# Kernel tuning notes

Measured on AMD Instinct MI355X. Metric: run time of the kernel, lower is better.

The kernel has to match this reference:

```python
import jax, jax.numpy as jnp
import numpy as np

N = 100_000
E = 1_600_000
IN, HID, OUT, ED = 128, 128, 64, 16
NEG_SLOPE = 0.2  # PyG GATConv default leaky_relu slope


def segment_softmax(logits, seg, num_segments):
    m = jax.ops.segment_max(logits, seg, num_segments=num_segments)
    m = jnp.where(jnp.isfinite(m), m, 0.0)
    e = jnp.exp(logits - m[seg])
    s = jax.ops.segment_sum(e, seg, num_segments=num_segments)
    return e / (s[seg] + 1e-16)


def gat_conv(x, edge_index, W, a_src, a_dst, b, edge_attr=None, We=None, ae=None):
    """PyG GATConv, heads=1, add_self_loops=True, fill_value='mean'."""
    n = x.shape[0]
    h = x @ W  # [N, C]
    loop = jnp.arange(n, dtype=edge_index.dtype)
    src = jnp.concatenate([edge_index[0], loop])  # [E+N]
    dst = jnp.concatenate([edge_index[1], loop])
    alpha = (h * a_src).sum(-1)[src] + (h * a_dst).sum(-1)[dst]  # [E+N]
    if edge_attr is not None:
        # self-loop edge_attr filled with per-destination mean (PyG fill_value='mean')
        cnt = jax.ops.segment_sum(jnp.ones((edge_attr.shape[0],), edge_attr.dtype), edge_index[1], num_segments=n)
        mean_attr = jax.ops.segment_sum(edge_attr, edge_index[1], num_segments=n) / jnp.maximum(cnt, 1.0)[:, None]
        ea = jnp.concatenate([edge_attr, mean_attr], axis=0)  # [E+N, ED]
        alpha = alpha + (ea @ We) @ ae
    alpha = jax.nn.leaky_relu(alpha, NEG_SLOPE)
    alpha = segment_softmax(alpha, dst, n)
    out = jax.ops.segment_sum(alpha[:, None] * h[src], dst, num_segments=n)  # scatter-add
    return out + b


def setup_inputs() -> dict:
    key = jax.random.key(0)
    ks = iter(jax.random.split(key, 32))
    g = lambda shape, fan: (jax.random.normal(next(ks), shape, jnp.float32) * (1.0 / np.sqrt(fan)))
    inp = {
        "x": jax.random.normal(next(ks), (N, IN), jnp.float32),
        "edge_index": jax.random.randint(next(ks), (2, E), 0, N, jnp.int32),
        "edge_attr": jax.random.normal(next(ks), (E, ED), jnp.float32),
        # conv1 (no edge_attr)
        "W1": g((IN, HID), IN), "a1_src": g((HID,), HID), "a1_dst": g((HID,), HID), "b1": jnp.zeros((HID,), jnp.float32),
        # conv2 (with edge_attr)
        "W2": g((HID, HID), HID), "a2_src": g((HID,), HID), "a2_dst": g((HID,), HID), "b2": jnp.zeros((HID,), jnp.float32),
        "We2": g((ED, HID), ED), "ae2": g((HID,), HID),
        # initial residual linear
        "Wr": g((IN, HID), IN), "br": jnp.zeros((HID,), jnp.float32),
        # conv_mu
        "Wmu": g((HID, OUT), HID), "amu_src": g((OUT,), OUT), "amu_dst": g((OUT,), OUT), "bmu": jnp.zeros((OUT,), jnp.float32),
        "Wemu": g((ED, OUT), ED), "aemu": g((OUT,), OUT),
        # conv_logstd
        "Wls": g((HID, OUT), HID), "als_src": g((OUT,), OUT), "als_dst": g((OUT,), OUT), "bls": jnp.zeros((OUT,), jnp.float32),
        "Wels": g((ED, OUT), ED), "aels": g((OUT,), OUT),
    }
    return inp


def reference(x, edge_index, edge_attr,
              W1, a1_src, a1_dst, b1,
              W2, a2_src, a2_dst, b2, We2, ae2,
              Wr, br,
              Wmu, amu_src, amu_dst, bmu, Wemu, aemu,
              Wls, als_src, als_dst, bls, Wels, aels):
    h = jax.nn.relu(gat_conv(x, edge_index, W1, a1_src, a1_dst, b1))
    h = jax.nn.relu(gat_conv(h, edge_index, W2, a2_src, a2_dst, b2, edge_attr, We2, ae2))
    h = h + (x @ Wr + br)  # initial residual
    mu = gat_conv(h, edge_index, Wmu, amu_src, amu_dst, bmu, edge_attr, Wemu, aemu)
    logstd = gat_conv(h, edge_index, Wls, als_src, als_dst, bls, edge_attr, Wels, aels)
    return mu, logstd
```

## Files before the change

kernel.cpp:

```cpp
#include <hip/hip_runtime.h>

#define NN 100000
#define NE 1600000
#define BSH 9
#define NBUK 196

typedef __attribute__((ext_vector_type(8))) short bf16x8;
typedef __attribute__((ext_vector_type(4))) float f32x4;

__device__ __forceinline__ float wave_sum(float v){
  #pragma unroll
  for (int o = 32; o; o >>= 1) v += __shfl_xor(v, o, 64);
  return v;
}
__device__ __forceinline__ float bf2f(unsigned short x){
  return __uint_as_float(((unsigned)x) << 16);
}
__device__ __forceinline__ unsigned short f2bf(float f){
  unsigned u = __float_as_uint(f);
  return (unsigned short)((u + 0x7FFFu + ((u >> 16) & 1u)) >> 16);
}
__device__ __forceinline__ float rl_f(float v, int j){
  return __uint_as_float(__builtin_amdgcn_readlane(__float_as_uint(v), j));
}

__global__ void prep_w_kernel(const float* __restrict__ W1, const float* __restrict__ W2,
                              const float* __restrict__ Wr, const float* __restrict__ Wmu,
                              const float* __restrict__ Wls,
                              unsigned short* __restrict__ W1t, unsigned short* __restrict__ W2t,
                              unsigned short* __restrict__ Wrt, unsigned short* __restrict__ Wmlt){
  int b = blockIdx.x, t = threadIdx.x;
  for (int it = 0; it < 64; it++){
    int idx = it*256 + t;
    int k = idx >> 7, c = idx & 127;
    float v; unsigned short* dst;
    if (b == 0){ v = W1[k*128+c]; dst = W1t; }
    else if (b == 1){ v = W2[k*128+c]; dst = W2t; }
    else if (b == 2){ v = Wr[k*128+c]; dst = Wrt; }
    else { v = (c & 1) ? Wls[k*64 + (c>>1)] : Wmu[k*64 + (c>>1)]; dst = Wmlt; }
    dst[c*128 + k] = f2bf(v);
  }
}

__global__ void wvec_kernel(const float* __restrict__ We2, const float* __restrict__ ae2,
                            const float* __restrict__ Wemu, const float* __restrict__ aemu,
                            const float* __restrict__ Wels, const float* __restrict__ aels,
                            float* __restrict__ wv){
  int t = threadIdx.x;
  if (t < 16){
    float s = 0.f; for (int c = 0; c < 128; c++) s += We2[t*128+c]*ae2[c];
    wv[t] = s;
  } else if (t < 32){
    int k = t-16; float s = 0.f; for (int c = 0; c < 64; c++) s += Wemu[k*64+c]*aemu[c];
    wv[16+k] = s;
  } else if (t < 48){
    int k = t-32; float s = 0.f; for (int c = 0; c < 64; c++) s += Wels[k*64+c]*aels[c];
    wv[32+k] = s;
  }
}

__global__ void cast_x_kernel(const float* __restrict__ x, unsigned short* __restrict__ Xb){
  int i = blockIdx.x*256 + threadIdx.x;
  if (i >= NN*128/8) return;
  const float4* src = (const float4*)x + (size_t)i*2;
  float4 v0 = src[0], v1 = src[1];
  ushort4 o0 = make_ushort4(f2bf(v0.x), f2bf(v0.y), f2bf(v0.z), f2bf(v0.w));
  ushort4 o1 = make_ushort4(f2bf(v1.x), f2bf(v1.y), f2bf(v1.z), f2bf(v1.w));
  *(ushort4*)(Xb + (size_t)i*8)     = o0;
  *(ushort4*)(Xb + (size_t)i*8 + 4) = o1;
}

__global__ void edge_scalar_kernel(const float* __restrict__ ea, const float* __restrict__ wv,
                                   float4* __restrict__ ew3){
  int e = blockIdx.x*256 + threadIdx.x;
  if (e >= NE) return;
  const float4* p = (const float4*)(ea + (size_t)e*16);
  float a[16]; float4 v;
  v = p[0]; a[0]=v.x; a[1]=v.y; a[2]=v.z; a[3]=v.w;
  v = p[1]; a[4]=v.x; a[5]=v.y; a[6]=v.z; a[7]=v.w;
  v = p[2]; a[8]=v.x; a[9]=v.y; a[10]=v.z; a[11]=v.w;
  v = p[3]; a[12]=v.x; a[13]=v.y; a[14]=v.z; a[15]=v.w;
  float s2 = 0.f, smu = 0.f, sls = 0.f;
  #pragma unroll
  for (int k = 0; k < 16; k++){
    s2  = fmaf(a[k], wv[k],    s2);
    smu = fmaf(a[k], wv[16+k], smu);
    sls = fmaf(a[k], wv[32+k], sls);
  }
  ew3[e] = make_float4(s2, smu, sls, 0.f);
}

__global__ void zero_kernel(int* __restrict__ p, int n){
  int i = blockIdx.x*256 + threadIdx.x;
  if (i < n) p[i] = 0;
}

__global__ __launch_bounds__(1024) void ehist_kernel(const int* __restrict__ ei,
                                                     unsigned* __restrict__ gbcnt){
  __shared__ unsigned h[256];
  int t = threadIdx.x;
  if (t < 256) h[t] = 0;
  __syncthreads();
  int e0 = blockIdx.x*4096 + t;
  #pragma unroll
  for (int k = 0; k < 4; k++){
    int e = e0 + k*1024;
    if (e < NE) atomicAdd(&h[ei[NE+e] >> BSH], 1);
  }
  __syncthreads();
  if (t < 256 && h[t]) atomicAdd(&gbcnt[t], h[t]);
}

__global__ void bscan_kernel(const unsigned* __restrict__ gbcnt,
                             unsigned* __restrict__ gbbase, int* __restrict__ rowptr){
  __shared__ unsigned sh[256];
  int t = threadIdx.x;
  unsigned v = gbcnt[t];
  sh[t] = v; __syncthreads();
  for (int o = 1; o < 256; o <<= 1){
    unsigned add = (t >= o) ? sh[t-o] : 0;
    __syncthreads();
    sh[t] += add;
    __syncthreads();
  }
  gbbase[t+1] = sh[t];
  if (t == 0){ gbbase[0] = 0; rowptr[NN] = NE; }
}

__global__ __launch_bounds__(1024) void bin_kernel(const int* __restrict__ ei,
                                                   const float4* __restrict__ ew3,
                                                   const unsigned* __restrict__ gbbase,
                                                   unsigned* __restrict__ gbfill,
                                                   uint2* __restrict__ bdu,
                                                   float4* __restrict__ bw){
  __shared__ unsigned hcnt[256], hbase[256], hcur[256];
  int t = threadIdx.x;
  if (t < 256){ hcnt[t] = 0; hcur[t] = 0; }
  __syncthreads();
  int d[4], u[4], b[4]; float4 w[4]; bool val[4];
  int e0 = blockIdx.x*4096 + t;
  #pragma unroll
  for (int k = 0; k < 4; k++){
    int e = e0 + k*1024;
    val[k] = e < NE;
    if (val[k]){
      d[k] = ei[NE+e]; u[k] = ei[e]; w[k] = ew3[e];
      b[k] = d[k] >> BSH;
      atomicAdd(&hcnt[b[k]], 1);
    }
  }
  __syncthreads();
  if (t < 256){
    unsigned c = hcnt[t];
    hbase[t] = c ? atomicAdd(&gbfill[t], c) : 0u;
  }
  __syncthreads();
  #pragma unroll
  for (int k = 0; k < 4; k++){
    if (val[k]){
      unsigned pos = atomicAdd(&hcur[b[k]], 1);
      unsigned slot = gbbase[b[k]] + hbase[b[k]] + pos;
      bdu[slot] = make_uint2((unsigned)d[k], (unsigned)u[k]);
      bw[slot]  = w[k];
    }
  }
}

__global__ __launch_bounds__(1024) void place_kernel(const uint2* __restrict__ bdu,
                                                     const float4* __restrict__ bw,
                                                     const unsigned* __restrict__ gbbase,
                                                     int* __restrict__ rowptr,
                                                     unsigned* __restrict__ csr_u,
                                                     float* __restrict__ ewp2,
                                                     float2* __restrict__ ewpmuls){
  __shared__ unsigned h[512], incl[512], cur[512];
  int b = blockIdx.x, t = threadIdx.x;
  unsigned cbase = gbbase[b];
  unsigned cnt = gbbase[b+1] - cbase;
  if (t < 512) h[t] = 0;
  __syncthreads();
  for (unsigned i = t; i < cnt; i += 1024)
    atomicAdd(&h[bdu[cbase+i].x & 511], 1);
  __syncthreads();
  if (t < 512) incl[t] = h[t];
  __syncthreads();
  for (int o = 1; o < 512; o <<= 1){
    unsigned add = (t >= o && t < 512) ? incl[t-o] : 0;
    __syncthreads();
    if (t < 512) incl[t] += add;
    __syncthreads();
  }
  if (t < 512){
    cur[t] = 0;
    int node = (b << BSH) + t;
    if (node < NN) rowptr[node] = (int)(cbase + incl[t] - h[t]);
  }
  __syncthreads();
  for (unsigned i = t; i < cnt; i += 1024){
    uint2 du = bdu[cbase+i];
    unsigned ld = du.x & 511;
    unsigned pos = atomicAdd(&cur[ld], 1);
    unsigned slot = cbase + (incl[ld] - h[ld]) + pos;
    float4 w = bw[cbase+i];
    csr_u[slot] = du.y;
    ewp2[slot] = w.x;
    ewpmuls[slot] = make_float2(w.y, w.z);
  }
}

template<bool OUTF32>
__global__ __launch_bounds__(256) void gemm_bf16(const unsigned short* __restrict__ Xb,
                                                 const unsigned short* __restrict__ Wt,
                                                 void* __restrict__ Y,
                                                 const float* __restrict__ bias, int nrows){
  __shared__ uint4 As[128*16];
  __shared__ uint4 Bs[128*16];
  int t = threadIdx.x;
  int row0 = blockIdx.x * 128;
  #pragma unroll
  for (int p = 0; p < 8; p++){
    int idx = p*256 + t;
    int r = idx >> 4, cir = idx & 15;
    uint4 v = make_uint4(0,0,0,0);
    if (row0 + r < nrows) v = *(const uint4*)(Xb + ((size_t)(row0+r))*128 + cir*8);
    As[r*16 + (cir ^ (r & 7))] = v;
  }
  #pragma unroll
  for (int p = 0; p < 8; p++){
    int idx = p*256 + t;
    int r = idx >> 4, cir = idx & 15;
    Bs[r*16 + (cir ^ (r & 7))] = *(const uint4*)(Wt + (size_t)r*128 + cir*8);
  }
  __syncthreads();
  int w = t >> 6, l = t & 63;
  int lr = l & 15;
  int lk = l >> 4;
  const bf16x8* As8 = (const bf16x8*)As;
  const bf16x8* Bs8 = (const bf16x8*)Bs;
  f32x4 acc[2][8];
  f32x4 zero = {0.f, 0.f, 0.f, 0.f};
  #pragma unroll
  for (int m = 0; m < 2; m++)
    #pragma unroll
    for (int n = 0; n < 8; n++) acc[m][n] = zero;
  #pragma unroll
  for (int ks = 0; ks < 4; ks++){
    bf16x8 a0, a1, bf[8];
    { int r = w*32 + lr;      a0 = As8[r*16 + ((ks*4+lk) ^ (r&7))]; }
    { int r = w*32 + 16 + lr; a1 = As8[r*16 + ((ks*4+lk) ^ (r&7))]; }
    #pragma unroll
    for (int nt = 0; nt < 8; nt++){
      int r = nt*16 + lr;
      bf[nt] = Bs8[r*16 + ((ks*4+lk) ^ (r&7))];
    }
    #pragma unroll
    for (int nt = 0; nt < 8; nt++){
      acc[0][nt] = __builtin_amdgcn_mfma_f32_16x16x32_bf16(a0, bf[nt], acc[0][nt], 0, 0, 0);
      acc[1][nt] = __builtin_amdgcn_mfma_f32_16x16x32_bf16(a1, bf[nt], acc[1][nt], 0, 0, 0);
    }
  }
  #pragma unroll
  for (int mt = 0; mt < 2; mt++){
    int gr0 = row0 + w*32 + mt*16 + lk*4;
    #pragma unroll
    for (int nt = 0; nt < 8; nt++){
      int col = nt*16 + lr;
      float bv = OUTF32 ? bias[col] : 0.f;
      #pragma unroll
      for (int i = 0; i < 4; i++){
        int r = gr0 + i;
        if (r < nrows){
          float o = acc[mt][nt][i];
          if constexpr (OUTF32) ((float*)Y)[(size_t)r*128 + col] = o + bv;
          else ((unsigned short*)Y)[(size_t)r*128 + col] = f2bf(o);
        }
      }
    }
  }
}

__global__ __launch_bounds__(256) void dots_kernel(const unsigned short* __restrict__ Hb,
                                                   const float* __restrict__ asrc,
                                                   const float* __restrict__ adst,
                                                   float* __restrict__ s, float* __restrict__ d){
  int n = (blockIdx.x * blockDim.x + threadIdx.x) >> 6;
  int lane = threadIdx.x & 63;
  if (n >= NN) return;
  ushort2 q = *(const ushort2*)(Hb + (size_t)n*128 + lane*2);
  float h0 = bf2f(q.x), h1 = bf2f(q.y);
  float ps = h0*asrc[lane*2] + h1*asrc[lane*2+1];
  float pd = h0*adst[lane*2] + h1*adst[lane*2+1];
  ps = wave_sum(ps); pd = wave_sum(pd);
  if (lane == 0){ s[n] = ps; d[n] = pd; }
}

__global__ __launch_bounds__(256) void dots_muls_kernel(const unsigned short* __restrict__ Yb,
                                                        const float* __restrict__ amus,
                                                        const float* __restrict__ amud,
                                                        const float* __restrict__ alss,
                                                        const float* __restrict__ alsd,
                                                        float2* __restrict__ sg,
                                                        float2* __restrict__ dg){
  int n = (blockIdx.x * blockDim.x + threadIdx.x) >> 6;
  int lane = threadIdx.x & 63;
  if (n >= NN) return;
  ushort2 q = *(const ushort2*)(Yb + (size_t)n*128 + lane*2);
  float hmu = bf2f(q.x), hls = bf2f(q.y);
  float smu = wave_sum(hmu * amus[lane]);
  float dmu = wave_sum(hmu * amud[lane]);
  float sls = wave_sum(hls * alss[lane]);
  float dls = wave_sum(hls * alsd[lane]);
  if (lane == 0){ sg[n] = make_float2(smu, sls); dg[n] = make_float2(dmu, dls); }
}

template<bool HAS_EW>
__global__ __launch_bounds__(256) void agg_conv(const unsigned short* __restrict__ Hb,
                                                const float* __restrict__ s,
                                                const float* __restrict__ dsc,
                                                const float* __restrict__ ewp,
                                                const int* __restrict__ rowptr,
                                                const unsigned* __restrict__ csr_u,
                                                const float* __restrict__ bias,
                                                const float* __restrict__ resid,
                                                unsigned short* __restrict__ out){
  int v = (blockIdx.x * blockDim.x + threadIdx.x) >> 6;
  int lane = threadIdx.x & 63;
  if (v >= NN) return;
  int rs = rowptr[v], re = rowptr[v+1];
  int deg = re - rs;
  float d_v = dsc[v];
  float pl = 0.f, acc0 = 0.f, acc1 = 0.f, ewl = 0.f;
  for (int base = rs; base < re; base += 64){
    int i = base + lane;
    int u = 0; float w = 0.f;
    if (i < re){
      u = (int)csr_u[i];
      float e = HAS_EW ? ewp[i] : 0.f;
      if (HAS_EW) ewl += e;
      float a = s[u] + d_v + e;
      float l = a > 0.f ? a : 0.2f*a;
      w = __expf(l);
    }
    pl += w;
    int nv = re - base; if (nv > 64) nv = 64;
    int j = 0;
    for (; j + 8 <= nv; j += 8){
      ushort2 q[8];
      float wj[8];
      #pragma unroll
      for (int k = 0; k < 8; k++){
        int uk = __builtin_amdgcn_readlane(u, j+k);
        wj[k] = rl_f(w, j+k);
        q[k] = *(const ushort2*)(Hb + (size_t)uk*128 + lane*2);
      }
      #pragma unroll
      for (int k = 0; k < 8; k++){
        acc0 = fmaf(wj[k], bf2f(q[k].x), acc0);
        acc1 = fmaf(wj[k], bf2f(q[k].y), acc1);
      }
    }
    for (; j < nv; j++){
      int uu = __builtin_amdgcn_readlane(u, j);
      float ww = rl_f(w, j);
      ushort2 q = *(const ushort2*)(Hb + (size_t)uu*128 + lane*2);
      acc0 = fmaf(ww, bf2f(q.x), acc0); acc1 = fmaf(ww, bf2f(q.y), acc1);
    }
  }
  float p = wave_sum(pl);
  float ews = HAS_EW ? wave_sum(ewl) : 0.f;
  float selfa = s[v] + d_v + (HAS_EW ? ews / (float)(deg > 1 ? deg : 1) : 0.f);
  float lself = selfa > 0.f ? selfa : 0.2f*selfa;
  float wself = __expf(lself);
  p += wself;
  {
    ushort2 q = *(const ushort2*)(Hb + (size_t)v*128 + lane*2);
    acc0 = fmaf(wself, bf2f(q.x), acc0);
    acc1 = fmaf(wself, bf2f(q.y), acc1);
  }
  float inv = 1.f / p;
  int c0 = lane*2;
  float o0 = acc0*inv + bias[c0], o1 = acc1*inv + bias[c0+1];
  o0 = fmaxf(o0, 0.f); o1 = fmaxf(o1, 0.f);
  if (HAS_EW){
    o0 += resid[(size_t)v*128 + c0];
    o1 += resid[(size_t)v*128 + c0 + 1];
  }
  *(ushort2*)(out + (size_t)v*128 + c0) = make_ushort2(f2bf(o0), f2bf(o1));
}

__global__ __launch_bounds__(256) void agg_muls(const unsigned short* __restrict__ Yb,
                                                const float2* __restrict__ sg,
                                                const float2* __restrict__ dg,
                                                const float2* __restrict__ ewpmuls,
                                                const int* __restrict__ rowptr,
                                                const unsigned* __restrict__ csr_u,
                                                const float* __restrict__ bmu,
                                                const float* __restrict__ bls,
                                                float* __restrict__ outmu,
                                                float* __restrict__ outls){
  int v = (blockIdx.x * blockDim.x + threadIdx.x) >> 6;
  int lane = threadIdx.x & 63;
  if (v >= NN) return;
  int rs = rowptr[v], re = rowptr[v+1];
  int deg = re - rs;
  float2 dv = dg[v];
  float pmu = 0.f, pls = 0.f, accmu = 0.f, accls = 0.f, ewlmu = 0.f, ewlls = 0.f;
  for (int base = rs; base < re; base += 64){
    int i = base + lane;
    int u = 0; float wmu = 0.f, wls = 0.f;
    if (i < re){
      u = (int)csr_u[i];
      float2 su = sg[u];
      float2 ee = ewpmuls[i];
      ewlmu += ee.x; ewlls += ee.y;
      float amu = su.x + dv.x + ee.x;
      float als = su.y + dv.y + ee.y;
      float lmu = amu > 0.f ? amu : 0.2f*amu;
      float lls = als > 0.f ? als : 0.2f*als;
      wmu = __expf(lmu); wls = __expf(lls);
    }
    pmu += wmu; pls += wls;
    int nv = re - base; if (nv > 64) nv = 64;
    int j = 0;
    for (; j + 8 <= nv; j += 8){
      ushort2 q[8];
      float wm[8], wl[8];
      #pragma unroll
      for (int k = 0; k < 8; k++){
        int uk = __builtin_amdgcn_readlane(u, j+k);
        wm[k] = rl_f(wmu, j+k);
        wl[k] = rl_f(wls, j+k);
        q[k] = *(const ushort2*)(Yb + (size_t)uk*128 + lane*2);
      }
      #pragma unroll
      for (int k = 0; k < 8; k++){
        accmu = fmaf(wm[k], bf2f(q[k].x), accmu);
        accls = fmaf(wl[k], bf2f(q[k].y), accls);
      }
    }
    for (; j < nv; j++){
      int uu = __builtin_amdgcn_readlane(u, j);
      float wmj = rl_f(wmu, j), wlj = rl_f(wls, j);
      ushort2 q = *(const ushort2*)(Yb + (size_t)uu*128 + lane*2);
      accmu = fmaf(wmj, bf2f(q.x), accmu);
      accls = fmaf(wlj, bf2f(q.y), accls);
    }
  }
  float Pmu = wave_sum(pmu), Pls = wave_sum(pls);
  float Emu = wave_sum(ewlmu), Els = wave_sum(ewlls);
  float2 sv = sg[v];
  float dnm = (float)(deg > 1 ? deg : 1);
  float selfmu = sv.x + dv.x + Emu/dnm;
  float selfls = sv.y + dv.y + Els/dnm;
  float lmu = selfmu > 0.f ? selfmu : 0.2f*selfmu;
  float lls = selfls > 0.f ? selfls : 0.2f*selfls;
  float wmu_s = __expf(lmu), wls_s = __expf(lls);
  Pmu += wmu_s; Pls += wls_s;
  {
    ushort2 q = *(const ushort2*)(Yb + (size_t)v*128 + lane*2);
    accmu = fmaf(wmu_s, bf2f(q.x), accmu);
    accls = fmaf(wls_s, bf2f(q.y), accls);
  }
  outmu[(size_t)v*64 + lane] = accmu/Pmu + bmu[lane];
  outls[(size_t)v*64 + lane] = accls/Pls + bls[lane];
}

extern "C" void kernel_launch(void* const* d_in, const int* in_sizes, int n_in,
                              void* d_out, int out_size, void* d_ws, size_t ws_size,
                              hipStream_t stream){
  const float* x    = (const float*)d_in[0];
  const int*   ei   = (const int*)  d_in[1];
  const float* ea   = (const float*)d_in[2];
  const float* W1   = (const float*)d_in[3];
  const float* a1s  = (const float*)d_in[4];
  const float* a1d  = (const float*)d_in[5];
  const float* b1   = (const float*)d_in[6];
  const float* W2   = (const float*)d_in[7];
  const float* a2s  = (const float*)d_in[8];
  const float* a2d  = (const float*)d_in[9];
  const float* b2   = (const float*)d_in[10];
  const float* We2  = (const float*)d_in[11];
  const float* ae2  = (const float*)d_in[12];
  const float* Wr   = (const float*)d_in[13];
  const float* br   = (const float*)d_in[14];
  const float* Wmu  = (const float*)d_in[15];
  const float* amus = (const float*)d_in[16];
  const float* amud = (const float*)d_in[17];
  const float* bmu  = (const float*)d_in[18];
  const float* Wemu = (const float*)d_in[19];
  const float* aemu = (const float*)d_in[20];
  const float* Wls  = (const float*)d_in[21];
  const float* alss = (const float*)d_in[22];
  const float* alsd = (const float*)d_in[23];
  const float* bls  = (const float*)d_in[24];
  const float* Wels = (const float*)d_in[25];
  const float* aels = (const float*)d_in[26];

  char* base = (char*)d_ws;
  size_t off = 0;
  auto alloc = [&](size_t bytes)->char*{
    char* p = base + off;
    off = (off + bytes + 511) & ~(size_t)511;
    return p;
  };
  float4*   ew3    = (float4*)alloc((size_t)NE*16);
  int*      rowptr = (int*)   alloc((size_t)(NN+1)*4);
  unsigned* gbcnt  = (unsigned*)alloc(512*4);
  unsigned* gbfill = gbcnt + 256;
  unsigned* gbbase = (unsigned*)alloc(257*4);
  uint2*    bdu    = (uint2*) alloc((size_t)NE*8);
  float4*   bw     = (float4*)alloc((size_t)NE*16);
  unsigned* csr_u  = (unsigned*)alloc((size_t)NE*4);
  float*    ewp2   = (float*) alloc((size_t)NE*4);
  float2*   ewpmls = (float2*)alloc((size_t)NE*8);
  float*    wv     = (float*) alloc(48*4);
  float*    s1     = (float*) alloc((size_t)NN*4);
  float*    d1     = (float*) alloc((size_t)NN*4);
  float2*   sg2    = (float2*)alloc((size_t)NN*8);
  float2*   dg2    = (float2*)alloc((size_t)NN*8);
  unsigned short* W1t  = (unsigned short*)alloc(128*128*2);
  unsigned short* W2t  = (unsigned short*)alloc(128*128*2);
  unsigned short* Wrt  = (unsigned short*)alloc(128*128*2);
  unsigned short* Wmlt = (unsigned short*)alloc(128*128*2);
  unsigned short* Xb   = (unsigned short*)alloc((size_t)NN*128*2);
  unsigned short* bufA = (unsigned short*)alloc((size_t)NN*128*2);
  unsigned short* bufB = (unsigned short*)alloc((size_t)NN*128*2);
  if (off > ws_size) return;

  float* outF = (float*)d_out;
  float* muO  = outF;
  float* lsO  = outF + (size_t)NN*64;

  const int EB  = (NE + 255)/256;
  const int HB  = (NE + 4095)/4096;
  const int WB  = (NN*64 + 255)/256;
  const int GB  = (NN + 127)/128;
  const int CB  = (NN*128/8 + 255)/256;

  prep_w_kernel<<<4, 256, 0, stream>>>(W1, W2, Wr, Wmu, Wls, W1t, W2t, Wrt, Wmlt);
  wvec_kernel<<<1, 64, 0, stream>>>(We2, ae2, Wemu, aemu, Wels, aels, wv);
  cast_x_kernel<<<CB, 256, 0, stream>>>(x, Xb);
  edge_scalar_kernel<<<EB, 256, 0, stream>>>(ea, wv, ew3);
  zero_kernel<<<2, 256, 0, stream>>>((int*)gbcnt, 512);
  ehist_kernel<<<HB, 1024, 0, stream>>>(ei, gbcnt);
  bscan_kernel<<<1, 256, 0, stream>>>(gbcnt, gbbase, rowptr);
  bin_kernel<<<HB, 1024, 0, stream>>>(ei, ew3, gbbase, gbfill, bdu, bw);
  place_kernel<<<NBUK, 1024, 0, stream>>>(bdu, bw, gbbase, rowptr, csr_u, ewp2, ewpmls);

  gemm_bf16<false><<<GB, 256, 0, stream>>>(Xb, W1t, bufA, nullptr, NN);
  dots_kernel<<<WB, 256, 0, stream>>>(bufA, a1s, a1d, s1, d1);
  agg_conv<false><<<WB, 256, 0, stream>>>(bufA, s1, d1, nullptr, rowptr, csr_u,
                                          b1, nullptr, bufB);
  gemm_bf16<false><<<GB, 256, 0, stream>>>(bufB, W2t, bufA, nullptr, NN);
  dots_kernel<<<WB, 256, 0, stream>>>(bufA, a2s, a2d, s1, d1);
  gemm_bf16<true><<<GB, 256, 0, stream>>>(Xb, Wrt, outF, br, NN);
  agg_conv<true><<<WB, 256, 0, stream>>>(bufA, s1, d1, ewp2, rowptr, csr_u,
                                         b2, outF, bufB);
  gemm_bf16<false><<<GB, 256, 0, stream>>>(bufB, Wmlt, bufA, nullptr, NN);
  dots_muls_kernel<<<WB, 256, 0, stream>>>(bufA, amus, amud, alss, alsd, sg2, dg2);
  agg_muls<<<WB, 256, 0, stream>>>(bufA, sg2, dg2, ewpmls, rowptr, csr_u,
                                   bmu, bls, muO, lsO);
}
```

Baseline: 515.8 us.

## Use 16-lane groups per node in aggregation and fuse edge-scalar into binning

```diff
diff --git a/kernel.cpp b/kernel.cpp
--- a/kernel.cpp
+++ b/kernel.cpp
@@ -13,15 +13,17 @@
   for (int o = 32; o; o >>= 1) v += __shfl_xor(v, o, 64);
   return v;
 }
+__device__ __forceinline__ float grp_sum16(float v){
+  #pragma unroll
+  for (int o = 8; o; o >>= 1) v += __shfl_xor(v, o, 16);
+  return v;
+}
 __device__ __forceinline__ float bf2f(unsigned short x){
   return __uint_as_float(((unsigned)x) << 16);
 }
 __device__ __forceinline__ unsigned short f2bf(float f){
   unsigned u = __float_as_uint(f);
   return (unsigned short)((u + 0x7FFFu + ((u >> 16) & 1u)) >> 16);
-}
-__device__ __forceinline__ float rl_f(float v, int j){
-  return __uint_as_float(__builtin_amdgcn_readlane(__float_as_uint(v), j));
 }
 
 __global__ void prep_w_kernel(const float* __restrict__ W1, const float* __restrict__ W2,
@@ -70,26 +72,6 @@
   *(ushort4*)(Xb + (size_t)i*8 + 4) = o1;
 }
 
-__global__ void edge_scalar_kernel(const float* __restrict__ ea, const float* __restrict__ wv,
-                                   float4* __restrict__ ew3){
-  int e = blockIdx.x*256 + threadIdx.x;
-  if (e >= NE) return;
-  const float4* p = (const float4*)(ea + (size_t)e*16);
-  float a[16]; float4 v;
-  v = p[0]; a[0]=v.x; a[1]=v.y; a[2]=v.z; a[3]=v.w;
-  v = p[1]; a[4]=v.x; a[5]=v.y; a[6]=v.z; a[7]=v.w;
-  v = p[2]; a[8]=v.x; a[9]=v.y; a[10]=v.z; a[11]=v.w;
-  v = p[3]; a[12]=v.x; a[13]=v.y; a[14]=v.z; a[15]=v.w;
-  float s2 = 0.f, smu = 0.f, sls = 0.f;
-  #pragma unroll
-  for (int k = 0; k < 16; k++){
-    s2  = fmaf(a[k], wv[k],    s2);
-    smu = fmaf(a[k], wv[16+k], smu);
-    sls = fmaf(a[k], wv[32+k], sls);
-  }
-  ew3[e] = make_float4(s2, smu, sls, 0.f);
-}
-
 __global__ void zero_kernel(int* __restrict__ p, int n){
   int i = blockIdx.x*256 + threadIdx.x;
   if (i < n) p[i] = 0;
@@ -128,14 +110,17 @@
 }
 
 __global__ __launch_bounds__(1024) void bin_kernel(const int* __restrict__ ei,
-                                                   const float4* __restrict__ ew3,
+                                                   const float* __restrict__ ea,
+                                                   const float* __restrict__ wv,
                                                    const unsigned* __restrict__ gbbase,
                                                    unsigned* __restrict__ gbfill,
                                                    uint2* __restrict__ bdu,
                                                    float4* __restrict__ bw){
   __shared__ unsigned hcnt[256], hbase[256], hcur[256];
+  __shared__ float wvs[48];
   int t = threadIdx.x;
   if (t < 256){ hcnt[t] = 0; hcur[t] = 0; }
+  else if (t >= 256 && t < 304) wvs[t-256] = wv[t-256];
   __syncthreads();
   int d[4], u[4], b[4]; float4 w[4]; bool val[4];
   int e0 = blockIdx.x*4096 + t;
@@ -144,9 +129,23 @@
     int e = e0 + k*1024;
     val[k] = e < NE;
     if (val[k]){
-      d[k] = ei[NE+e]; u[k] = ei[e]; w[k] = ew3[e];
+      d[k] = ei[NE+e]; u[k] = ei[e];
       b[k] = d[k] >> BSH;
       atomicAdd(&hcnt[b[k]], 1);
+      const float4* p = (const float4*)(ea + (size_t)e*16);
+      float a[16]; float4 vv;
+      vv = p[0]; a[0]=vv.x; a[1]=vv.y; a[2]=vv.z; a[3]=vv.w;
+      vv = p[1]; a[4]=vv.x; a[5]=vv.y; a[6]=vv.z; a[7]=vv.w;
+      vv = p[2]; a[8]=vv.x; a[9]=vv.y; a[10]=vv.z; a[11]=vv.w;
+      vv = p[3]; a[12]=vv.x; a[13]=vv.y; a[14]=vv.z; a[15]=vv.w;
+      float s2 = 0.f, smu = 0.f, sls = 0.f;
+      #pragma unroll
+      for (int q = 0; q < 16; q++){
+        s2  = fmaf(a[q], wvs[q],    s2);
+        smu = fmaf(a[q], wvs[16+q], smu);
+        sls = fmaf(a[q], wvs[32+q], sls);
+      }
+      w[k] = make_float4(s2, smu, sls, 0.f);
     }
   }
   __syncthreads();
@@ -323,15 +322,16 @@
                                                 const float* __restrict__ bias,
                                                 const float* __restrict__ resid,
                                                 unsigned short* __restrict__ out){
-  int v = (blockIdx.x * blockDim.x + threadIdx.x) >> 6;
-  int lane = threadIdx.x & 63;
+  int v = (blockIdx.x * blockDim.x + threadIdx.x) >> 4;
+  int lig = threadIdx.x & 15;
   if (v >= NN) return;
   int rs = rowptr[v], re = rowptr[v+1];
   int deg = re - rs;
   float d_v = dsc[v];
-  float pl = 0.f, acc0 = 0.f, acc1 = 0.f, ewl = 0.f;
-  for (int base = rs; base < re; base += 64){
-    int i = base + lane;
+  float acc[8] = {0.f,0.f,0.f,0.f,0.f,0.f,0.f,0.f};
+  float pl = 0.f, ewl = 0.f;
+  for (int base = rs; base < re; base += 16){
+    int i = base + lig;
     int u = 0; float w = 0.f;
     if (i < re){
       u = (int)csr_u[i];
@@ -342,50 +342,73 @@
       w = __expf(l);
     }
     pl += w;
-    int nv = re - base; if (nv > 64) nv = 64;
+    int nv = re - base; if (nv > 16) nv = 16;
     int j = 0;
-    for (; j + 8 <= nv; j += 8){
-      ushort2 q[8];
-      float wj[8];
-      #pragma unroll
-      for (int k = 0; k < 8; k++){
-        int uk = __builtin_amdgcn_readlane(u, j+k);
-        wj[k] = rl_f(w, j+k);
-        q[k] = *(const ushort2*)(Hb + (size_t)uk*128 + lane*2);
-      }
-      #pragma unroll
-      for (int k = 0; k < 8; k++){
-        acc0 = fmaf(wj[k], bf2f(q[k].x), acc0);
-        acc1 = fmaf(wj[k], bf2f(q[k].y), acc1);
+    for (; j + 4 <= nv; j += 4){
+      uint4 q[4]; float wj[4];
+      #pragma unroll
+      for (int k = 0; k < 4; k++){
+        int uk = __shfl(u, j+k, 16);
+        wj[k] = __shfl(w, j+k, 16);
+        q[k] = *(const uint4*)(Hb + (size_t)uk*128 + lig*8);
+      }
+      #pragma unroll
+      for (int k = 0; k < 4; k++){
+        const unsigned* qq = (const unsigned*)&q[k];
+        #pragma unroll
+        for (int c = 0; c < 4; c++){
+          acc[2*c]   = fmaf(wj[k], __uint_as_float(qq[c] << 16), acc[2*c]);
+          acc[2*c+1] = fmaf(wj[k], __uint_as_float(qq[c] & 0xFFFF0000u), acc[2*c+1]);
+        }
       }
     }
     for (; j < nv; j++){
-      int uu = __builtin_amdgcn_readlane(u, j);
-      float ww = rl_f(w, j);
-      ushort2 q = *(const ushort2*)(Hb + (size_t)uu*128 + lane*2);
-      acc0 = fmaf(ww, bf2f(q.x), acc0); acc1 = fmaf(ww, bf2f(q.y), acc1);
-    }
-  }
-  float p = wave_sum(pl);
-  float ews = HAS_EW ? wave_sum(ewl) : 0.f;
+      int uk = __shfl(u, j, 16);
+      float wk = __shfl(w, j, 16);
+      uint4 q = *(const uint4*)(Hb + (size_t)uk*128 + lig*8);
+      const unsigned* qq = (const unsigned*)&q;
+      #pragma unroll
+      for (int c = 0; c < 4; c++){
+        acc[2*c]   = fmaf(wk, __uint_as_float(qq[c] << 16), acc[2*c]);
+        acc[2*c+1] = fmaf(wk, __uint_as_float(qq[c] & 0xFFFF0000u), acc[2*c+1]);
+      }
+    }
+  }
+  float p = grp_sum16(pl);
+  float ews = HAS_EW ? grp_sum16(ewl) : 0.f;
   float selfa = s[v] + d_v + (HAS_EW ? ews / (float)(deg > 1 ? deg : 1) : 0.f);
   float lself = selfa > 0.f ? selfa : 0.2f*selfa;
   float wself = __expf(lself);
   p += wself;
   {
-    ushort2 q = *(const ushort2*)(Hb + (size_t)v*128 + lane*2);
-    acc0 = fmaf(wself, bf2f(q.x), acc0);
-    acc1 = fmaf(wself, bf2f(q.y), acc1);
+    uint4 q = *(const uint4*)(Hb + (size_t)v*128 + lig*8);
+    const unsigned* qq = (const unsigned*)&q;
+    #pragma unroll
+    for (int c = 0; c < 4; c++){
+      acc[2*c]   = fmaf(wself, __uint_as_float(qq[c] << 16), acc[2*c]);
+      acc[2*c+1] = fmaf(wself, __uint_as_float(qq[c] & 0xFFFF0000u), acc[2*c+1]);
+    }
   }
   float inv = 1.f / p;
-  int c0 = lane*2;
-  float o0 = acc0*inv + bias[c0], o1 = acc1*inv + bias[c0+1];
-  o0 = fmaxf(o0, 0.f); o1 = fmaxf(o1, 0.f);
+  int c0 = lig*8;
+  float o[8];
+  #pragma unroll
+  for (int c = 0; c < 8; c++){
+    o[c] = acc[c]*inv + bias[c0+c];
+    o[c] = fmaxf(o[c], 0.f);
+  }
   if (HAS_EW){
-    o0 += resid[(size_t)v*128 + c0];
-    o1 += resid[(size_t)v*128 + c0 + 1];
-  }
-  *(ushort2*)(out + (size_t)v*128 + c0) = make_ushort2(f2bf(o0), f2bf(o1));
+    float4 r0 = *(const float4*)(resid + (size_t)v*128 + c0);
+    float4 r1 = *(const float4*)(resid + (size_t)v*128 + c0 + 4);
+    o[0]+=r0.x; o[1]+=r0.y; o[2]+=r0.z; o[3]+=r0.w;
+    o[4]+=r1.x; o[5]+=r1.y; o[6]+=r1.z; o[7]+=r1.w;
+  }
+  uint4 ow;
+  unsigned* owp = (unsigned*)&ow;
+  #pragma unroll
+  for (int c = 0; c < 4; c++)
+    owp[c] = (unsigned)f2bf(o[2*c]) | ((unsigned)f2bf(o[2*c+1]) << 16);
+  *(uint4*)(out + (size_t)v*128 + c0) = ow;
 }
 
 __global__ __launch_bounds__(256) void agg_muls(const unsigned short* __restrict__ Yb,
@@ -398,15 +421,16 @@
                                                 const float* __restrict__ bls,
                                                 float* __restrict__ outmu,
                                                 float* __restrict__ outls){
-  int v = (blockIdx.x * blockDim.x + threadIdx.x) >> 6;
-  int lane = threadIdx.x & 63;
+  int v = (blockIdx.x * blockDim.x + threadIdx.x) >> 4;
+  int lig = threadIdx.x & 15;
   if (v >= NN) return;
   int rs = rowptr[v], re = rowptr[v+1];
   int deg = re - rs;
   float2 dv = dg[v];
-  float pmu = 0.f, pls = 0.f, accmu = 0.f, accls = 0.f, ewlmu = 0.f, ewlls = 0.f;
-  for (int base = rs; base < re; base += 64){
-    int i = base + lane;
+  float accmu[4] = {0.f,0.f,0.f,0.f}, accls[4] = {0.f,0.f,0.f,0.f};
+  float pmu = 0.f, pls = 0.f, ewlmu = 0.f, ewlls = 0.f;
+  for (int base = rs; base < re; base += 16){
+    int i = base + lig;
     int u = 0; float wmu = 0.f, wls = 0.f;
     if (i < re){
       u = (int)csr_u[i];
@@ -420,34 +444,41 @@
       wmu = __expf(lmu); wls = __expf(lls);
     }
     pmu += wmu; pls += wls;
-    int nv = re - base; if (nv > 64) nv = 64;
+    int nv = re - base; if (nv > 16) nv = 16;
     int j = 0;
-    for (; j + 8 <= nv; j += 8){
-      ushort2 q[8];
-      float wm[8], wl[8];
-      #pragma unroll
-      for (int k = 0; k < 8; k++){
-        int uk = __builtin_amdgcn_readlane(u, j+k);
-        wm[k] = rl_f(wmu, j+k);
-        wl[k] = rl_f(wls, j+k);
-        q[k] = *(const ushort2*)(Yb + (size_t)uk*128 + lane*2);
-      }
-      #pragma unroll
-      for (int k = 0; k < 8; k++){
-        accmu = fmaf(wm[k], bf2f(q[k].x), accmu);
-        accls = fmaf(wl[k], bf2f(q[k].y), accls);
+    for (; j + 4 <= nv; j += 4){
+      uint4 q[4]; float wm[4], wl[4];
+      #pragma unroll
+      for (int k = 0; k < 4; k++){
+        int uk = __shfl(u, j+k, 16);
+        wm[k] = __shfl(wmu, j+k, 16);
+        wl[k] = __shfl(wls, j+k, 16);
+        q[k] = *(const uint4*)(Yb + (size_t)uk*128 + lig*8);
+      }
+      #pragma unroll
+      for (int k = 0; k < 4; k++){
+        const unsigned* qq = (const unsigned*)&q[k];
+        #pragma unroll
+        for (int c = 0; c < 4; c++){
+          accmu[c] = fmaf(wm[k], __uint_as_float(qq[c] << 16), accmu[c]);
+          accls[c] = fmaf(wl[k], __uint_as_float(qq[c] & 0xFFFF0000u), accls[c]);
+        }
       }
     }
     for (; j < nv; j++){
-      int uu = __builtin_amdgcn_readlane(u, j);
-      float wmj = rl_f(wmu, j), wlj = rl_f(wls, j);
-      ushort2 q = *(const ushort2*)(Yb + (size_t)uu*128 + lane*2);
-      accmu = fmaf(wmj, bf2f(q.x), accmu);
-      accls = fmaf(wlj, bf2f(q.y), accls);
-    }
-  }
-  float Pmu = wave_sum(pmu), Pls = wave_sum(pls);
-  float Emu = wave_sum(ewlmu), Els = wave_sum(ewlls);
+      int uk = __shfl(u, j, 16);
+      float wmk = __shfl(wmu, j, 16), wlk = __shfl(wls, j, 16);
+      uint4 q = *(const uint4*)(Yb + (size_t)uk*128 + lig*8);
+      const unsigned* qq = (const unsigned*)&q;
+      #pragma unroll
+      for (int c = 0; c < 4; c++){
+        accmu[c] = fmaf(wmk, __uint_as_float(qq[c] << 16), accmu[c]);
+        accls[c] = fmaf(wlk, __uint_as_float(qq[c] & 0xFFFF0000u), accls[c]);
+      }
+    }
+  }
+  float Pmu = grp_sum16(pmu), Pls = grp_sum16(pls);
+  float Emu = grp_sum16(ewlmu), Els = grp_sum16(ewlls);
   float2 sv = sg[v];
   float dnm = (float)(deg > 1 ? deg : 1);
   float selfmu = sv.x + dv.x + Emu/dnm;
@@ -457,12 +488,22 @@
   float wmu_s = __expf(lmu), wls_s = __expf(lls);
   Pmu += wmu_s; Pls += wls_s;
   {
-    ushort2 q = *(const ushort2*)(Yb + (size_t)v*128 + lane*2);
-    accmu = fmaf(wmu_s, bf2f(q.x), accmu);
-    accls = fmaf(wls_s, bf2f(q.y), accls);
-  }
-  outmu[(size_t)v*64 + lane] = accmu/Pmu + bmu[lane];
-  outls[(size_t)v*64 + lane] = accls/Pls + bls[lane];
+    uint4 q = *(const uint4*)(Yb + (size_t)v*128 + lig*8);
+    const unsigned* qq = (const unsigned*)&q;
+    #pragma unroll
+    for (int c = 0; c < 4; c++){
+      accmu[c] = fmaf(wmu_s, __uint_as_float(qq[c] << 16), accmu[c]);
+      accls[c] = fmaf(wls_s, __uint_as_float(qq[c] & 0xFFFF0000u), accls[c]);
+    }
+  }
+  float imu = 1.f/Pmu, ils = 1.f/Pls;
+  int c0 = lig*4;
+  float4 omu = make_float4(accmu[0]*imu + bmu[c0], accmu[1]*imu + bmu[c0+1],
+                           accmu[2]*imu + bmu[c0+2], accmu[3]*imu + bmu[c0+3]);
+  float4 ols = make_float4(accls[0]*ils + bls[c0], accls[1]*ils + bls[c0+1],
+                           accls[2]*ils + bls[c0+2], accls[3]*ils + bls[c0+3]);
+  *(float4*)(outmu + (size_t)v*64 + c0) = omu;
+  *(float4*)(outls + (size_t)v*64 + c0) = ols;
 }
 
 extern "C" void kernel_launch(void* const* d_in, const int* in_sizes, int n_in,
@@ -503,7 +544,6 @@
     off = (off + bytes + 511) & ~(size_t)511;
     return p;
   };
-  float4*   ew3    = (float4*)alloc((size_t)NE*16);
   int*      rowptr = (int*)   alloc((size_t)(NN+1)*4);
   unsigned* gbcnt  = (unsigned*)alloc(512*4);
   unsigned* gbfill = gbcnt + 256;
@@ -531,33 +571,32 @@
   float* muO  = outF;
   float* lsO  = outF + (size_t)NN*64;
 
-  const int EB  = (NE + 255)/256;
-  const int HB  = (NE + 4095)/4096;
-  const int WB  = (NN*64 + 255)/256;
-  const int GB  = (NN + 127)/128;
-  const int CB  = (NN*128/8 + 255)/256;
+  const int HB   = (NE + 4095)/4096;
+  const int WB   = (NN*64 + 255)/256;
+  const int WB16 = (NN*16 + 255)/256;
+  const int GB   = (NN + 127)/128;
+  const int CB   = (NN*128/8 + 255)/256;
 
   prep_w_kernel<<<4, 256, 0, stream>>>(W1, W2, Wr, Wmu, Wls, W1t, W2t, Wrt, Wmlt);
   wvec_kernel<<<1, 64, 0, stream>>>(We2, ae2, Wemu, aemu, Wels, aels, wv);
   cast_x_kernel<<<CB, 256, 0, stream>>>(x, Xb);
-  edge_scalar_kernel<<<EB, 256, 0, stream>>>(ea, wv, ew3);
   zero_kernel<<<2, 256, 0, stream>>>((int*)gbcnt, 512);
   ehist_kernel<<<HB, 1024, 0, stream>>>(ei, gbcnt);
   bscan_kernel<<<1, 256, 0, stream>>>(gbcnt, gbbase, rowptr);
-  bin_kernel<<<HB, 1024, 0, stream>>>(ei, ew3, gbbase, gbfill, bdu, bw);
+  bin_kernel<<<HB, 1024, 0, stream>>>(ei, ea, wv, gbbase, gbfill, bdu, bw);
   place_kernel<<<NBUK, 1024, 0, stream>>>(bdu, bw, gbbase, rowptr, csr_u, ewp2, ewpmls);
 
   gemm_bf16<false><<<GB, 256, 0, stream>>>(Xb, W1t, bufA, nullptr, NN);
   dots_kernel<<<WB, 256, 0, stream>>>(bufA, a1s, a1d, s1, d1);
-  agg_conv<false><<<WB, 256, 0, stream>>>(bufA, s1, d1, nullptr, rowptr, csr_u,
-                                          b1, nullptr, bufB);
+  agg_conv<false><<<WB16, 256, 0, stream>>>(bufA, s1, d1, nullptr, rowptr, csr_u,
+                                            b1, nullptr, bufB);
   gemm_bf16<false><<<GB, 256, 0, stream>>>(bufB, W2t, bufA, nullptr, NN);
   dots_kernel<<<WB, 256, 0, stream>>>(bufA, a2s, a2d, s1, d1);
   gemm_bf16<true><<<GB, 256, 0, stream>>>(Xb, Wrt, outF, br, NN);
-  agg_conv<true><<<WB, 256, 0, stream>>>(bufA, s1, d1, ewp2, rowptr, csr_u,
-                                         b2, outF, bufB);
+  agg_conv<true><<<WB16, 256, 0, stream>>>(bufA, s1, d1, ewp2, rowptr, csr_u,
+                                           b2, outF, bufB);
   gemm_bf16<false><<<GB, 256, 0, stream>>>(bufB, Wmlt, bufA, nullptr, NN);
   dots_muls_kernel<<<WB, 256, 0, stream>>>(bufA, amus, amud, alss, alsd, sg2, dg2);
-  agg_muls<<<WB, 256, 0, stream>>>(bufA, sg2, dg2, ewpmls, rowptr, csr_u,
-                                   bmu, bls, muO, lsO);
-}
+  agg_muls<<<WB16, 256, 0, stream>>>(bufA, sg2, dg2, ewpmls, rowptr, csr_u,
+                                     bmu, bls, muO, lsO);
+}
```

Measured after the change: 490.6 us. -4.9%, faster.
